# Kernel tuning notes

Hardware: AMD Instinct MI355X
Metric: run time of the kernel (lower is better)

## Reference

```python
import jax, jax.numpy as jnp
import numpy as np

B, L, P, C = 8, 4, 1024, 256
NH, NS = 8, 4
HD = C // NH  # 32
LEVEL_HW = [(64, 64), (32, 32), (16, 16), (8, 8)]


def setup_inputs() -> dict:
    key = jax.random.key(0)
    ks = jax.random.split(key, 14)
    inp = {
        "x": jax.random.normal(ks[0], (B, L, P, C), jnp.float32),
        # reference points are grid_sample coords in [-1, 1]
        "ref": jax.random.uniform(ks[1], (B, L, P, 2), jnp.float32, -0.9, 0.9),
    }
    for i, (h, w) in enumerate(LEVEL_HW):
        inp[f"feat{i}"] = jax.random.normal(ks[2 + i], (B, C, h, w), jnp.float32)
    inp["w_attn"] = jax.random.normal(ks[6], (C, NH * NS), jnp.float32) * 0.02
    inp["b_attn"] = jax.random.normal(ks[7], (NH * NS,), jnp.float32) * 0.02
    inp["w_off"] = jax.random.normal(ks[8], (C, 2 * NH * NS), jnp.float32) * 0.02
    inp["b_off"] = jax.random.normal(ks[9], (2 * NH * NS,), jnp.float32) * 0.02
    inp["embed_w"] = jax.random.normal(ks[10], (L, C, HD), jnp.float32) * 0.02
    inp["embed_b"] = jax.random.normal(ks[11], (L, HD), jnp.float32) * 0.02
    return inp


def grid_sample_bilinear(feat, grid):
    """torch.F.grid_sample(mode='bilinear', padding_mode='zeros', align_corners=True).
    feat: (B, C, H, W); grid: (B, Gh, Gw, 2) with (x, y) in [-1, 1].
    Returns (B, Gh, Gw, C)  (already permuted vs torch's (B, C, Gh, Gw))."""
    Bn, Cn, H, W = feat.shape
    fx = (grid[..., 0] + 1.0) * 0.5 * (W - 1)  # align_corners=True mapping
    fy = (grid[..., 1] + 1.0) * 0.5 * (H - 1)
    x0f = jnp.floor(fx)
    y0f = jnp.floor(fy)
    x0 = x0f.astype(jnp.int32)
    y0 = y0f.astype(jnp.int32)
    x1 = x0 + 1
    y1 = y0 + 1
    wx1 = fx - x0f
    wy1 = fy - y0f
    wx0 = 1.0 - wx1
    wy0 = 1.0 - wy1
    feat_hwc = jnp.transpose(feat, (0, 2, 3, 1))  # (B, H, W, C)

    def gather(yi, xi):
        valid = ((yi >= 0) & (yi < H) & (xi >= 0) & (xi < W)).astype(feat.dtype)
        yc = jnp.clip(yi, 0, H - 1)
        xc = jnp.clip(xi, 0, W - 1)
        v = jax.vmap(lambda f, y, x: f[y, x])(feat_hwc, yc, xc)  # (B, Gh, Gw, C)
        return v * valid[..., None]

    out = (gather(y0, x0) * (wy0 * wx0)[..., None]
           + gather(y0, x1) * (wy0 * wx1)[..., None]
           + gather(y1, x0) * (wy1 * wx0)[..., None]
           + gather(y1, x1) * (wy1 * wx1)[..., None])
    return out


def reference(x, ref, feat0, feat1, feat2, feat3,
              w_attn, b_attn, w_off, b_off, embed_w, embed_b):
    feats = [feat0, feat1, feat2, feat3]
    b, l, p, c = x.shape
    # attention weights: softmax over samples
    weights = jax.nn.softmax((x @ w_attn + b_attn).reshape(b, l, p, NH, NS), axis=-1)
    # sampling offsets, squashed by tanh
    offsets = jnp.tanh((x @ w_off + b_off).reshape(b, l, p, NH * NS, 2))
    pos = offsets + ref[:, :, :, None, :]  # (b, l, p, NH*NS, 2)
    sampled = []
    for i, f in enumerate(feats):
        s = grid_sample_bilinear(f, pos[:, i])  # (b, p, NH*NS, C_l)
        sampled.append(s @ embed_w[i] + embed_b[i])  # (b, p, NH*NS, HD)
    fs = jnp.stack(sampled, axis=1).reshape(b, l, p, NH, NS, HD)
    out = (weights[..., None] * fs).sum(axis=-2).reshape(b, l, p, NH * HD)
    return out
```

## Files before the change

kernel.cpp:

```cpp
#include <hip/hip_runtime.h>
#include <math.h>

#define B_   8
#define L_   4
#define P_   1024
#define C_   256
#define NH_  8
#define NS_  4
#define HD_  32

typedef _Float16 half8 __attribute__((ext_vector_type(8)));
typedef float    f32x4 __attribute__((ext_vector_type(4)));

#define G_F     0u
#define SAMP_F  1392640u
#define WU_F    5586944u
#define ET_F    5611520u

__constant__ const int kGoff[4] = {0, 1048576, 1310720, 1376256};

#define XH2 72
#define LGS 100
#define NG_GPROJ 680

__global__ void k0_conv(const float* __restrict__ wa, const float* __restrict__ wo,
                        const float* __restrict__ embed_w,
                        _Float16* __restrict__ WuT, _Float16* __restrict__ ET16) {
  const int bx = blockIdx.x, t = threadIdx.x;
  if (bx < 96) {
    const int n = bx;
    const float v = (n < 32) ? wa[t * 32 + n] : wo[t * 64 + (n - 32)];
    WuT[n * 256 + t] = (_Float16)v;
  } else {
    const int i0 = (bx - 96) * 1024 + t * 4;
    const int l = i0 >> 13, rem = i0 & 8191;
    const int c = rem >> 5, e0 = rem & 31;
    const float4 v = *(const float4*)(embed_w + i0);
    _Float16* d = ET16 + l * 8192 + c;
    d[(e0 + 0) * 256] = (_Float16)v.x;
    d[(e0 + 1) * 256] = (_Float16)v.y;
    d[(e0 + 2) * 256] = (_Float16)v.z;
    d[(e0 + 3) * 256] = (_Float16)v.w;
  }
}

__global__ __launch_bounds__(256) void stage1(
    const float* __restrict__ f0, const float* __restrict__ f1,
    const float* __restrict__ f2, const float* __restrict__ f3,
    const _Float16* __restrict__ ET16, _Float16* __restrict__ g16,
    const float* __restrict__ x,
    const float* __restrict__ ref,
    const _Float16* __restrict__ WuT,
    const float* __restrict__ ba, const float* __restrict__ bo,
    float4* __restrict__ samp4)
{
  __shared__ float4 smraw4[1600];
  const int t = threadIdx.x;
  const int bx = blockIdx.x;
  const int lane = t & 63, wv = t >> 6;
  const int lr = lane & 15, kg = lane >> 4;

  if (bx < NG_GPROJ) {
    const int b = bx / 85;
    int sub = bx - b * 85, l, tile;
    const float* src;
    if (sub < 64)      { l = 0; tile = sub;      src = f0; }
    else if (sub < 80) { l = 1; tile = sub - 64; src = f1; }
    else if (sub < 84) { l = 2; tile = sub - 80; src = f2; }
    else               { l = 3; tile = 0;        src = f3; }
    const int Wl = 64 >> l, S = Wl * Wl;
    const int s0 = tile * 64;
    const int srow = s0 + wv * 16 + lr;

    const float* sb = src + (size_t)b * C_ * S + srow;
    const _Float16* ETl = ET16 + (size_t)l * 8192;

    f32x4 acc0 = (f32x4){0.f, 0.f, 0.f, 0.f};
    f32x4 acc1 = (f32x4){0.f, 0.f, 0.f, 0.f};

    float vc[8], vn[8];
    #pragma unroll
    for (int i = 0; i < 8; ++i) vn[i] = sb[(size_t)(kg * 8 + i) * S];

    #pragma unroll
    for (int c = 0; c < 8; ++c) {
      const int c0 = c * 32;
      #pragma unroll
      for (int i = 0; i < 8; ++i) vc[i] = vn[i];
      if (c < 7) {
        #pragma unroll
        for (int i = 0; i < 8; ++i)
          vn[i] = sb[(size_t)(c0 + 32 + kg * 8 + i) * S];
      }
      const half8 a = {(_Float16)vc[0], (_Float16)vc[1], (_Float16)vc[2], (_Float16)vc[3],
                       (_Float16)vc[4], (_Float16)vc[5], (_Float16)vc[6], (_Float16)vc[7]};
      const half8 b0 = *(const half8*)(ETl + (size_t)lr * 256 + c0 + kg * 8);
      const half8 b1 = *(const half8*)(ETl + (size_t)(16 + lr) * 256 + c0 + kg * 8);
      acc0 = __builtin_amdgcn_mfma_f32_16x16x32_f16(a, b0, acc0, 0, 0, 0);
      acc1 = __builtin_amdgcn_mfma_f32_16x16x32_f16(a, b1, acc1, 0, 0, 0);
    }

    _Float16* gb = g16 + kGoff[l] + ((size_t)b * S + s0 + wv * 16 + kg * 4) * 32;
    #pragma unroll
    for (int r = 0; r < 4; ++r) {
      gb[r * 32 + lr]      = (_Float16)acc0[r];
      gb[r * 32 + 16 + lr] = (_Float16)acc1[r];
    }
    return;
  }

  _Float16* smx = (_Float16*)smraw4;
  _Float16* smw = (_Float16*)smraw4 + 64 * XH2;
  float*    lg  = (float*)smraw4;

  const int blk = bx - NG_GPROJ;
  const int gp0 = blk * 64;

  f32x4 acc[6];
  #pragma unroll
  for (int nt = 0; nt < 6; ++nt) acc[nt] = (f32x4){0.f, 0.f, 0.f, 0.f};

  #pragma unroll
  for (int chunk = 0; chunk < 4; ++chunk) {
    const int c0 = chunk * 64;
    if (chunk) __syncthreads();
    {
      const int pt = t >> 2, q = t & 3;
      const float4* src = (const float4*)(x + (size_t)(gp0 + pt) * 256 + c0 + q * 16);
      const float4 v0 = src[0], v1 = src[1], v2 = src[2], v3 = src[3];
      _Float16* dst = smx + pt * XH2 + q * 16;
      *(half8*)dst = (half8){(_Float16)v0.x, (_Float16)v0.y, (_Float16)v0.z, (_Float16)v0.w,
                             (_Float16)v1.x, (_Float16)v1.y, (_Float16)v1.z, (_Float16)v1.w};
      *(half8*)(dst + 8) = (half8){(_Float16)v2.x, (_Float16)v2.y, (_Float16)v2.z, (_Float16)v2.w,
                                   (_Float16)v3.x, (_Float16)v3.y, (_Float16)v3.z, (_Float16)v3.w};
    }
    {
      #pragma unroll
      for (int q = 0; q < 3; ++q) {
        const int idx = q * 256 + t;
        const int n = idx >> 3, col8 = idx & 7;
        *(float4*)(smw + n * XH2 + col8 * 8) =
            *(const float4*)(WuT + (size_t)n * 256 + c0 + col8 * 8);
      }
    }
    __syncthreads();

    #pragma unroll
    for (int ks = 0; ks < 2; ++ks) {
      const half8 a = *(const half8*)(smx + (wv * 16 + lr) * XH2 + ks * 32 + kg * 8);
      #pragma unroll
      for (int nt = 0; nt < 6; ++nt) {
        const half8 bf = *(const half8*)(smw + (nt * 16 + lr) * XH2 + ks * 32 + kg * 8);
        acc[nt] = __builtin_amdgcn_mfma_f32_16x16x32_f16(a, bf, acc[nt], 0, 0, 0);
      }
    }
  }
  __syncthreads();

  #pragma unroll
  for (int nt = 0; nt < 6; ++nt) {
    const int n = nt * 16 + lr;
    const float bv = (n < 32) ? ba[n] : bo[n - 32];
    #pragma unroll
    for (int r = 0; r < 4; ++r)
      lg[(wv * 16 + kg * 4 + r) * LGS + n] = acc[nt][r] + bv;
  }
  __syncthreads();

  #pragma unroll
  for (int k = 0; k < 8; ++k) {
    const int slot = k * 256 + t;
    const int pp = slot >> 5, j = slot & 31;
    const int gp = gp0 + pp;
    const int l = (gp >> 10) & 3;
    const int Wl = 64 >> l;
    const float* lgp = lg + pp * LGS;
    const int h4 = (j >> 2) * 4;
    const float l0 = lgp[h4], l1 = lgp[h4 + 1], l2 = lgp[h4 + 2], l3 = lgp[h4 + 3];
    const float m = fmaxf(fmaxf(l0, l1), fmaxf(l2, l3));
    const float e0 = expf(l0 - m), e1 = expf(l1 - m), e2 = expf(l2 - m), e3 = expf(l3 - m);
    const float inv = 1.f / (e0 + e1 + e2 + e3);
    const float es[4] = {e0, e1, e2, e3};
    const float wj = es[j & 3] * inv;
    const float ox = tanhf(lgp[32 + 2 * j])     + ref[(size_t)gp * 2];
    const float oy = tanhf(lgp[32 + 2 * j + 1]) + ref[(size_t)gp * 2 + 1];
    const float sc = 0.5f * (float)(Wl - 1);
    samp4[(size_t)gp * 32 + j] = make_float4(wj, (ox + 1.f) * sc, (oy + 1.f) * sc, 0.f);
  }
}

__global__ __launch_bounds__(256) void k3_main(
    const _Float16* __restrict__ g16,
    const float4* __restrict__ samp4,
    const float* __restrict__ embed_b,
    float* __restrict__ out)
{
  __shared__ int4   tofs[256];
  __shared__ float4 tws[256];
  const int t = threadIdx.x, blk = blockIdx.x;
  const int gp0 = blk * 8;
  const int l = (gp0 >> 10) & 3, b = gp0 >> 12;
  const int Wl = 64 >> l;
  const int gbase = kGoff[l] + b * Wl * Wl * 32;

  {
    const float4 s = samp4[(size_t)gp0 * 32 + t];
    const float fx = s.y, fy = s.z;
    const float x0f = floorf(fx), y0f = floorf(fy);
    const int x0 = (int)x0f, y0 = (int)y0f, x1 = x0 + 1, y1 = y0 + 1;
    const float wx1 = fx - x0f, wy1 = fy - y0f;
    const float wx0 = 1.f - wx1, wy0 = 1.f - wy1;
    const float xv0 = (x0 >= 0 && x0 < Wl) ? 1.f : 0.f;
    const float xv1 = (x1 >= 0 && x1 < Wl) ? 1.f : 0.f;
    const float yv0 = (y0 >= 0 && y0 < Wl) ? 1.f : 0.f;
    const float yv1 = (y1 >= 0 && y1 < Wl) ? 1.f : 0.f;
    const int x0c = min(max(x0, 0), Wl - 1), x1c = min(max(x1, 0), Wl - 1);
    const int y0c = min(max(y0, 0), Wl - 1), y1c = min(max(y1, 0), Wl - 1);
    tofs[t] = make_int4(gbase + (y0c * Wl + x0c) * 32,
                        gbase + (y0c * Wl + x1c) * 32,
                        gbase + (y1c * Wl + x0c) * 32,
                        gbase + (y1c * Wl + x1c) * 32);
    const float w = s.x;
    tws[t] = make_float4(w * wy0 * wx0 * yv0 * xv0,
                         w * wy0 * wx1 * yv0 * xv1,
                         w * wy1 * wx0 * yv1 * xv0,
                         w * wy1 * wx1 * yv1 * xv1);
  }
  __syncthreads();

  const int dq = t & 3, h = (t >> 2) & 7, pt = t >> 5;
  float a[8];
  {
    const float4* bb = (const float4*)(embed_b + l * 32 + dq * 8);
    const float4 b0 = bb[0], b1 = bb[1];
    a[0] = b0.x; a[1] = b0.y; a[2] = b0.z; a[3] = b0.w;
    a[4] = b1.x; a[5] = b1.y; a[6] = b1.z; a[7] = b1.w;
  }
  #pragma unroll
  for (int s = 0; s < 4; ++s) {
    const int slot = pt * 32 + h * 4 + s;
    const int4   o = tofs[slot];
    const float4 w = tws[slot];
    const half8 v00 = *(const half8*)(g16 + o.x + dq * 8);
    const half8 v01 = *(const half8*)(g16 + o.y + dq * 8);
    const half8 v10 = *(const half8*)(g16 + o.z + dq * 8);
    const half8 v11 = *(const half8*)(g16 + o.w + dq * 8);
    #pragma unroll
    for (int j = 0; j < 8; ++j)
      a[j] += w.x * (float)v00[j] + w.y * (float)v01[j]
            + w.z * (float)v10[j] + w.w * (float)v11[j];
  }
  float* od = out + (size_t)(gp0 + pt) * 256 + h * 32 + dq * 8;
  ((float4*)od)[0] = make_float4(a[0], a[1], a[2], a[3]);
  ((float4*)od)[1] = make_float4(a[4], a[5], a[6], a[7]);
}

extern "C" void kernel_launch(void* const* d_in, const int* in_sizes, int n_in,
                              void* d_out, int out_size, void* d_ws, size_t ws_size,
                              hipStream_t stream) {
  const float* x      = (const float*)d_in[0];
  const float* ref    = (const float*)d_in[1];
  const float* w_attn = (const float*)d_in[6];
  const float* b_attn = (const float*)d_in[7];
  const float* w_off  = (const float*)d_in[8];
  const float* b_off  = (const float*)d_in[9];
  const float* emb_w  = (const float*)d_in[10];
  const float* emb_b  = (const float*)d_in[11];
  float* ws  = (float*)d_ws;
  float* out = (float*)d_out;

  _Float16* g16   = (_Float16*)(ws + G_F);
  float4*   samp4 = (float4*)(ws + SAMP_F);
  _Float16* WuT   = (_Float16*)(ws + WU_F);
  _Float16* ET16  = (_Float16*)(ws + ET_F);

  k0_conv<<<128, 256, 0, stream>>>(w_attn, w_off, emb_w, WuT, ET16);

  stage1<<<NG_GPROJ + B_ * L_ * P_ / 64, 256, 0, stream>>>(
      (const float*)d_in[2], (const float*)d_in[3],
      (const float*)d_in[4], (const float*)d_in[5], ET16, g16,
      x, ref, WuT, b_attn, b_off, samp4);

  k3_main<<<B_ * L_ * P_ / 8, 256, 0, stream>>>(g16, samp4, emb_b, out);
}
```

Measured before the change: 50.59 us.

## Load x fragments directly into registers and halve stage1 shared memory footprint

The projection part of stage1 now loads each wave's x rows straight from global memory into half8 MFMA A-fragments held in registers, instead of staging them through shared memory every chunk. Only the weight tile stays in LDS. The logits buffer is processed in two halves of 32 points, so shared memory shrinks from 25.6KB to 13.8KB, which can allow more resident blocks. In exchange it uses more registers for the fragments, adds an extra barrier round, and the x global loads are strided per lane, which may coalesce less well.

```diff
diff --git a/kernel.cpp b/kernel.cpp
--- a/kernel.cpp
+++ b/kernel.cpp
@@ -54,7 +54,7 @@
     const float* __restrict__ ba, const float* __restrict__ bo,
     float4* __restrict__ samp4)
 {
-  __shared__ float4 smraw4[1600];
+  __shared__ char smraw[13824];
   const int t = threadIdx.x;
   const int bx = blockIdx.x;
   const int lane = t & 63, wv = t >> 6;
@@ -109,12 +109,21 @@
     return;
   }
 
-  _Float16* smx = (_Float16*)smraw4;
-  _Float16* smw = (_Float16*)smraw4 + 64 * XH2;
-  float*    lg  = (float*)smraw4;
+  _Float16* smw = (_Float16*)smraw;
+  float*    lg32 = (float*)smraw;
 
   const int blk = bx - NG_GPROJ;
   const int gp0 = blk * 64;
+
+  const float* xrow = x + (size_t)(gp0 + wv * 16 + lr) * 256;
+  half8 af[8];
+  #pragma unroll
+  for (int f = 0; f < 8; ++f) {
+    const float4* p = (const float4*)(xrow + f * 32 + kg * 8);
+    const float4 u = p[0], w2 = p[1];
+    af[f] = (half8){(_Float16)u.x,  (_Float16)u.y,  (_Float16)u.z,  (_Float16)u.w,
+                    (_Float16)w2.x, (_Float16)w2.y, (_Float16)w2.z, (_Float16)w2.w};
+  }
 
   f32x4 acc[6];
   #pragma unroll
@@ -124,16 +133,6 @@
   for (int chunk = 0; chunk < 4; ++chunk) {
     const int c0 = chunk * 64;
     if (chunk) __syncthreads();
-    {
-      const int pt = t >> 2, q = t & 3;
-      const float4* src = (const float4*)(x + (size_t)(gp0 + pt) * 256 + c0 + q * 16);
-      const float4 v0 = src[0], v1 = src[1], v2 = src[2], v3 = src[3];
-      _Float16* dst = smx + pt * XH2 + q * 16;
-      *(half8*)dst = (half8){(_Float16)v0.x, (_Float16)v0.y, (_Float16)v0.z, (_Float16)v0.w,
-                             (_Float16)v1.x, (_Float16)v1.y, (_Float16)v1.z, (_Float16)v1.w};
-      *(half8*)(dst + 8) = (half8){(_Float16)v2.x, (_Float16)v2.y, (_Float16)v2.z, (_Float16)v2.w,
-                                   (_Float16)v3.x, (_Float16)v3.y, (_Float16)v3.z, (_Float16)v3.w};
-    }
     {
       #pragma unroll
       for (int q = 0; q < 3; ++q) {
@@ -147,7 +146,7 @@
 
     #pragma unroll
     for (int ks = 0; ks < 2; ++ks) {
-      const half8 a = *(const half8*)(smx + (wv * 16 + lr) * XH2 + ks * 32 + kg * 8);
+      const half8 a = af[chunk * 2 + ks];
       #pragma unroll
       for (int nt = 0; nt < 6; ++nt) {
         const half8 bf = *(const half8*)(smw + (nt * 16 + lr) * XH2 + ks * 32 + kg * 8);
@@ -158,34 +157,40 @@
   __syncthreads();
 
   #pragma unroll
-  for (int nt = 0; nt < 6; ++nt) {
-    const int n = nt * 16 + lr;
-    const float bv = (n < 32) ? ba[n] : bo[n - 32];
-    #pragma unroll
-    for (int r = 0; r < 4; ++r)
-      lg[(wv * 16 + kg * 4 + r) * LGS + n] = acc[nt][r] + bv;
-  }
-  __syncthreads();
-
-  #pragma unroll
-  for (int k = 0; k < 8; ++k) {
-    const int slot = k * 256 + t;
-    const int pp = slot >> 5, j = slot & 31;
-    const int gp = gp0 + pp;
-    const int l = (gp >> 10) & 3;
-    const int Wl = 64 >> l;
-    const float* lgp = lg + pp * LGS;
-    const int h4 = (j >> 2) * 4;
-    const float l0 = lgp[h4], l1 = lgp[h4 + 1], l2 = lgp[h4 + 2], l3 = lgp[h4 + 3];
-    const float m = fmaxf(fmaxf(l0, l1), fmaxf(l2, l3));
-    const float e0 = expf(l0 - m), e1 = expf(l1 - m), e2 = expf(l2 - m), e3 = expf(l3 - m);
-    const float inv = 1.f / (e0 + e1 + e2 + e3);
-    const float es[4] = {e0, e1, e2, e3};
-    const float wj = es[j & 3] * inv;
-    const float ox = tanhf(lgp[32 + 2 * j])     + ref[(size_t)gp * 2];
-    const float oy = tanhf(lgp[32 + 2 * j + 1]) + ref[(size_t)gp * 2 + 1];
-    const float sc = 0.5f * (float)(Wl - 1);
-    samp4[(size_t)gp * 32 + j] = make_float4(wj, (ox + 1.f) * sc, (oy + 1.f) * sc, 0.f);
+  for (int half = 0; half < 2; ++half) {
+    if ((wv >> 1) == half) {
+      #pragma unroll
+      for (int nt = 0; nt < 6; ++nt) {
+        const int n = nt * 16 + lr;
+        const float bv = (n < 32) ? ba[n] : bo[n - 32];
+        #pragma unroll
+        for (int r = 0; r < 4; ++r)
+          lg32[((wv & 1) * 16 + kg * 4 + r) * LGS + n] = acc[nt][r] + bv;
+      }
+    }
+    __syncthreads();
+
+    #pragma unroll
+    for (int k = 0; k < 4; ++k) {
+      const int slot = k * 256 + t;
+      const int ppl = slot >> 5, j = slot & 31;
+      const int gp = gp0 + half * 32 + ppl;
+      const int l = (gp >> 10) & 3;
+      const int Wl = 64 >> l;
+      const float* lgp = lg32 + ppl * LGS;
+      const int h4 = (j >> 2) * 4;
+      const float l0 = lgp[h4], l1 = lgp[h4 + 1], l2 = lgp[h4 + 2], l3 = lgp[h4 + 3];
+      const float m = fmaxf(fmaxf(l0, l1), fmaxf(l2, l3));
+      const float e0 = expf(l0 - m), e1 = expf(l1 - m), e2 = expf(l2 - m), e3 = expf(l3 - m);
+      const float inv = 1.f / (e0 + e1 + e2 + e3);
+      const float es[4] = {e0, e1, e2, e3};
+      const float wj = es[j & 3] * inv;
+      const float ox = tanhf(lgp[32 + 2 * j])     + ref[(size_t)gp * 2];
+      const float oy = tanhf(lgp[32 + 2 * j + 1]) + ref[(size_t)gp * 2 + 1];
+      const float sc = 0.5f * (float)(Wl - 1);
+      samp4[(size_t)gp * 32 + j] = make_float4(wj, (ox + 1.f) * sc, (oy + 1.f) * sc, 0.f);
+    }
+    if (half == 0) __syncthreads();
   }
 }
 
```

Result: slower. 52.12 us (+3.0%).
